# Performance work log

Hardware: AMD Instinct MI355X
Metric: run time of the kernel (lower is better)

## Reference

```python
import jax, jax.numpy as jnp
import numpy as np

N_NODES = 50000
N_EDGES = 800000
D_FEAT = 64
EDGE_DIM = 64


def setup_inputs() -> dict:
    key = jax.random.key(0)
    k1, k2, k3, k4 = jax.random.split(key, 4)
    node_feats = jax.random.normal(k1, (N_NODES, D_FEAT), dtype=jnp.float32)
    senders = jax.random.randint(k2, (N_EDGES,), 0, N_NODES, dtype=jnp.int32)
    receivers = jax.random.randint(k3, (N_EDGES,), 0, N_NODES, dtype=jnp.int32)
    # Dense(edge_dim) applied to concat([recv, send]) of width 2*D_FEAT
    W = jax.random.normal(k4, (2 * D_FEAT, EDGE_DIM), dtype=jnp.float32) / np.sqrt(2.0 * D_FEAT)
    b = jnp.zeros((EDGE_DIM,), dtype=jnp.float32)
    return {"node_feats": node_feats, "senders": senders, "receivers": receivers, "W": W, "b": b}


def reference(node_feats, senders, receivers, W, b):
    # gather node features at each edge endpoint: [E, D]
    feats_send = node_feats[senders]
    feats_recv = node_feats[receivers]
    # concat(recv, send) -> [E, 2D], Dense + tanh -> [E, edge_dim]
    edge_feats = jnp.concatenate([feats_recv, feats_send], axis=-1)
    return jnp.tanh(edge_feats @ W + b)
```

## Files before the change

kernel.cpp:

```cpp
#include <hip/hip_runtime.h>

#define N_EDGES 800000
#define D 64

typedef __attribute__((ext_vector_type(8))) short bf16x8;
typedef __attribute__((ext_vector_type(4))) float f32x4;

__device__ __forceinline__ short f2bf(float f) {
    unsigned int u = __float_as_uint(f);
    u += 0x7fffu + ((u >> 16) & 1u);
    return (short)(u >> 16);
}

__global__ __launch_bounds__(256) void edge_mlp(
    const float* __restrict__ node_feats,
    const int*   __restrict__ senders,
    const int*   __restrict__ receivers,
    const float* __restrict__ W,
    const float* __restrict__ bias,
    float*       __restrict__ out)
{
    const int lane = threadIdx.x & 63;
    const int m    = lane & 15;
    const int q    = lane >> 4;
    const long wid = (long)blockIdx.x * 4 + (threadIdx.x >> 6);
    const long e0  = wid * 64;
    if (e0 >= N_EDGES) return;

    int nidx[2][4];
#pragma unroll
    for (int mt = 0; mt < 4; ++mt) {
        const long e = e0 + mt * 16 + m;
        nidx[0][mt] = receivers[e];
        nidx[1][mt] = senders[e];
    }

    f32x4 acc[4][4];
#pragma unroll
    for (int mt = 0; mt < 4; ++mt)
#pragma unroll
        for (int nt = 0; nt < 4; ++nt)
            acc[mt][nt] = (f32x4)0.0f;

#pragma unroll
    for (int ki = 0; ki < 4; ++ki) {
        const int k0 = ki * 32 + q * 8;

        bf16x8 bfrag[4];
        const float* wp = W + (long)k0 * D + m;
#pragma unroll
        for (int nt = 0; nt < 4; ++nt) {
#pragma unroll
            for (int j = 0; j < 8; ++j)
                bfrag[nt][j] = f2bf(wp[j * D + nt * 16]);
        }

#pragma unroll
        for (int mt = 0; mt < 4; ++mt) {
            const int node = nidx[ki >> 1][mt];
            const float* fp = node_feats + (long)node * D + (k0 & 63);
            const float4 lo = *(const float4*)fp;
            const float4 hi = *(const float4*)(fp + 4);
            bf16x8 afrag;
            afrag[0] = f2bf(lo.x); afrag[1] = f2bf(lo.y);
            afrag[2] = f2bf(lo.z); afrag[3] = f2bf(lo.w);
            afrag[4] = f2bf(hi.x); afrag[5] = f2bf(hi.y);
            afrag[6] = f2bf(hi.z); afrag[7] = f2bf(hi.w);
#pragma unroll
            for (int nt = 0; nt < 4; ++nt)
                acc[mt][nt] = __builtin_amdgcn_mfma_f32_16x16x32_bf16(
                    afrag, bfrag[nt], acc[mt][nt], 0, 0, 0);
        }
    }

    float bv[4];
#pragma unroll
    for (int nt = 0; nt < 4; ++nt) bv[nt] = bias[nt * 16 + m];

#pragma unroll
    for (int mt = 0; mt < 4; ++mt) {
#pragma unroll
        for (int r = 0; r < 4; ++r) {
            const long row = e0 + mt * 16 + q * 4 + r;
            float* op = out + row * D + m;
#pragma unroll
            for (int nt = 0; nt < 4; ++nt) {
                const float x  = acc[mt][nt][r] + bv[nt];
                const float ax = __builtin_fabsf(x);
                const float t  = __expf(-2.0f * ax);
                float y = (1.0f - t) * __builtin_amdgcn_rcpf(1.0f + t);
                y = __builtin_copysignf(y, x);
                __builtin_nontemporal_store(y, op + nt * 16);
            }
        }
    }
}

extern "C" void kernel_launch(void* const* d_in, const int* in_sizes, int n_in,
                              void* d_out, int out_size, void* d_ws, size_t ws_size,
                              hipStream_t stream) {
    const float* node_feats = (const float*)d_in[0];
    const int*   senders    = (const int*)d_in[1];
    const int*   receivers  = (const int*)d_in[2];
    const float* W          = (const float*)d_in[3];
    const float* bias       = (const float*)d_in[4];
    float*       out        = (float*)d_out;

    const int n_blocks = (N_EDGES + 255) / 256;
    edge_mlp<<<n_blocks, 256, 0, stream>>>(node_feats, senders, receivers, W, bias, out);
}
```

Baseline: 287.6 us.

## Pre-convert node features and transposed weights to bf16 in a prep kernel

Adds a prep kernel that converts the node feature table to bf16 once and writes a transposed, padded bf16 copy of W into workspace. The edge kernel then gathers 16-byte bf16 rows and loads weight fragments directly, with no per-edge float-to-bf16 conversion and no strided scalar weight loads. This halves the bytes per gathered row and removes repeated conversion ALU work, at the cost of an extra kernel launch and one pass over the 12.8MB feature table.

```diff
diff --git a/kernel.cpp b/kernel.cpp
--- a/kernel.cpp
+++ b/kernel.cpp
@@ -1,22 +1,51 @@
 #include <hip/hip_runtime.h>
 
 #define N_EDGES 800000
+#define N_NODES 50000
 #define D 64
+#define WT_STRIDE 136
 
 typedef __attribute__((ext_vector_type(8))) short bf16x8;
 typedef __attribute__((ext_vector_type(4))) float f32x4;
 
-__device__ __forceinline__ short f2bf(float f) {
+__device__ __forceinline__ unsigned short f2bf(float f) {
     unsigned int u = __float_as_uint(f);
     u += 0x7fffu + ((u >> 16) & 1u);
-    return (short)(u >> 16);
+    return (unsigned short)(u >> 16);
+}
+__device__ __forceinline__ unsigned int pack2(float a, float b) {
+    return (unsigned int)f2bf(a) | ((unsigned int)f2bf(b) << 16);
+}
+
+__global__ __launch_bounds__(256) void prep(
+    const float* __restrict__ nf, const float* __restrict__ W,
+    unsigned short* __restrict__ nodes_bf, unsigned short* __restrict__ wt_bf)
+{
+    if (blockIdx.x == gridDim.x - 1) {
+        for (int i = threadIdx.x; i < D * 128; i += 256) {
+            const int n = i >> 7, k = i & 127;
+            wt_bf[n * WT_STRIDE + k] = f2bf(W[k * D + n]);
+        }
+    } else {
+        const long base = ((long)blockIdx.x * 256 + threadIdx.x) * 8;
+        if (base < (long)N_NODES * D) {
+            const float4 lo = *(const float4*)(nf + base);
+            const float4 hi = *(const float4*)(nf + base + 4);
+            uint4 p;
+            p.x = pack2(lo.x, lo.y);
+            p.y = pack2(lo.z, lo.w);
+            p.z = pack2(hi.x, hi.y);
+            p.w = pack2(hi.z, hi.w);
+            *(uint4*)(nodes_bf + base) = p;
+        }
+    }
 }
 
 __global__ __launch_bounds__(256) void edge_mlp(
-    const float* __restrict__ node_feats,
+    const unsigned short* __restrict__ nodes_bf,
+    const unsigned short* __restrict__ wt_bf,
     const int*   __restrict__ senders,
     const int*   __restrict__ receivers,
-    const float* __restrict__ W,
     const float* __restrict__ bias,
     float*       __restrict__ out)
 {
@@ -47,30 +76,23 @@
         const int k0 = ki * 32 + q * 8;
 
         bf16x8 bfrag[4];
-        const float* wp = W + (long)k0 * D + m;
 #pragma unroll
-        for (int nt = 0; nt < 4; ++nt) {
+        for (int nt = 0; nt < 4; ++nt)
+            bfrag[nt] = *(const bf16x8*)(wt_bf + (nt * 16 + m) * WT_STRIDE + k0);
+
+        bf16x8 afrag[4];
 #pragma unroll
-            for (int j = 0; j < 8; ++j)
-                bfrag[nt][j] = f2bf(wp[j * D + nt * 16]);
+        for (int mt = 0; mt < 4; ++mt) {
+            const int node = nidx[ki >> 1][mt];
+            afrag[mt] = *(const bf16x8*)(nodes_bf + node * D + (k0 & 63));
         }
 
 #pragma unroll
-        for (int mt = 0; mt < 4; ++mt) {
-            const int node = nidx[ki >> 1][mt];
-            const float* fp = node_feats + (long)node * D + (k0 & 63);
-            const float4 lo = *(const float4*)fp;
-            const float4 hi = *(const float4*)(fp + 4);
-            bf16x8 afrag;
-            afrag[0] = f2bf(lo.x); afrag[1] = f2bf(lo.y);
-            afrag[2] = f2bf(lo.z); afrag[3] = f2bf(lo.w);
-            afrag[4] = f2bf(hi.x); afrag[5] = f2bf(hi.y);
-            afrag[6] = f2bf(hi.z); afrag[7] = f2bf(hi.w);
+        for (int mt = 0; mt < 4; ++mt)
 #pragma unroll
             for (int nt = 0; nt < 4; ++nt)
                 acc[mt][nt] = __builtin_amdgcn_mfma_f32_16x16x32_bf16(
-                    afrag, bfrag[nt], acc[mt][nt], 0, 0, 0);
-        }
+                    afrag[mt], bfrag[nt], acc[mt][nt], 0, 0, 0);
     }
 
     float bv[4];
@@ -106,6 +128,12 @@
     const float* bias       = (const float*)d_in[4];
     float*       out        = (float*)d_out;
 
+    unsigned short* nodes_bf = (unsigned short*)d_ws;
+    unsigned short* wt_bf    = (unsigned short*)((char*)d_ws + (size_t)N_NODES * D * 2);
+
+    const int node_blocks = ((N_NODES * D / 8) + 255) / 256;
+    prep<<<node_blocks + 1, 256, 0, stream>>>(node_feats, W, nodes_bf, wt_bf);
+
     const int n_blocks = (N_EDGES + 255) / 256;
-    edge_mlp<<<n_blocks, 256, 0, stream>>>(node_feats, senders, receivers, W, bias, out);
+    edge_mlp<<<n_blocks, 256, 0, stream>>>(nodes_bf, wt_bf, senders, receivers, bias, out);
 }
```

Measured after the change: 274.3 us. 4.6% less time.
